# Optimization experiments

Hardware: AMD Instinct MI355X
Metric: run time of the kernel (lower is better)

## Reference

```python
import jax, jax.numpy as jnp
import numpy as np
import math

N, E, IN, OUT, H = 50000, 200000, 128, 128, 4
EPS = 1e-5
NEG_SLOPE = 0.01


def _ln(a):
    m = jnp.mean(a, axis=-1, keepdims=True)
    v = jnp.mean((a - m) ** 2, axis=-1, keepdims=True)
    return (a - m) / jnp.sqrt(v + EPS)


def setup_inputs() -> dict:
    key = jax.random.key(0)
    ks = jax.random.split(key, 24)
    glorot = lambda k, shape: jax.random.uniform(k, shape, jnp.float32,
                                                 -math.sqrt(6.0 / (shape[-2] + shape[-1])),
                                                 math.sqrt(6.0 / (shape[-2] + shape[-1])))
    lin = lambda k, fan_in, shape: jax.random.uniform(k, shape, jnp.float32,
                                                      -1.0 / math.sqrt(fan_in), 1.0 / math.sqrt(fan_in))
    inp = {
        "x": jax.random.normal(ks[0], (N, IN), jnp.float32),
        "edge_index": jax.random.randint(ks[1], (2, E), 0, N, jnp.int32),
        "edge_feature": jax.random.normal(ks[2], (E, IN), jnp.float32),
        # per-head projection matrices [H, IN, OUT]
        "Kv2v": glorot(ks[3], (H, IN, OUT)),
        "Ke2v": glorot(ks[4], (H, IN, OUT)),
        "Vv2v": glorot(ks[5], (H, IN, OUT)),
        "Ve2v": glorot(ks[6], (H, IN, OUT)),
        # per-head linear_update: [H, 2*OUT, 2*OUT]
        "lu_W": lin(ks[7], 2 * OUT, (H, 2 * OUT, 2 * OUT)),
        "lu_b": lin(ks[8], 2 * OUT, (H, 2 * OUT)),
        "ln1_g": jnp.ones((H, 2 * OUT), jnp.float32),
        "ln1_b": jnp.zeros((H, 2 * OUT), jnp.float32),
        # per-head msg_layer linear: [H, 2*OUT, OUT]
        "msg_W": lin(ks[9], 2 * OUT, (H, 2 * OUT, OUT)),
        "msg_b": lin(ks[10], 2 * OUT, (H, OUT)),
        "ln2_g": jnp.ones((H, OUT), jnp.float32),
        "ln2_b": jnp.zeros((H, OUT), jnp.float32),
        # concat projection [OUT*H, OUT]
        "cat_W": lin(ks[11], OUT * H, (OUT * H, OUT)),
        "cat_b": lin(ks[12], OUT * H, (OUT,)),
        # input projection [IN, OUT]
        "inp_W": lin(ks[13], IN, (IN, OUT)),
        "inp_b": lin(ks[14], IN, (OUT,)),
        # batchnorm affine
        "bn_g": jnp.ones((OUT,), jnp.float32),
        "bn_b": jnp.zeros((OUT,), jnp.float32),
    }
    return inp


def reference(x, edge_index, edge_feature, Kv2v, Ke2v, Vv2v, Ve2v,
              lu_W, lu_b, ln1_g, ln1_b, msg_W, msg_b, ln2_g, ln2_b,
              cat_W, cat_b, inp_W, inp_b, bn_g, bn_b):
    src, dst = edge_index[0], edge_index[1]  # j -> i
    scale = 1.0 / math.sqrt(2 * OUT)
    heads = []
    for h in range(H):  # small fixed loop over structurally distinct heads
        Kv = x @ Kv2v[h]            # [N, OUT]
        Vv = x @ Vv2v[h]
        KE = edge_feature @ Ke2v[h]  # [E, OUT]
        VE = edge_feature @ Ve2v[h]
        q_i = Kv[dst]                # [E, OUT]
        query = jnp.concatenate([q_i, q_i], axis=1)          # [E, 2*OUT]
        key_j = jnp.concatenate([Kv[src], KE], axis=1)       # [E, 2*OUT]
        alpha = query * key_j * scale
        val = jnp.concatenate([Vv[src], VE], axis=1)         # [E, 2*OUT]
        gate = jax.nn.sigmoid(_ln(alpha) * ln1_g[h] + ln1_b[h])
        m = (val @ lu_W[h] + lu_b[h]) * gate                 # [E, 2*OUT]
        m = m @ msg_W[h] + msg_b[h]                          # [E, OUT]
        m = _ln(m) * ln2_g[h] + ln2_b[h]
        m = jax.nn.leaky_relu(m, NEG_SLOPE)
        heads.append(jax.ops.segment_sum(m, dst, num_segments=N))  # [N, OUT]
    hv = jnp.concatenate(heads, axis=1)          # [N, OUT*H]
    out = hv @ cat_W + cat_b                      # [N, OUT]
    mu = jnp.mean(out, axis=0)
    var = jnp.mean((out - mu) ** 2, axis=0)      # biased, training-mode BN
    out = (out - mu) / jnp.sqrt(var + EPS) * bn_g + bn_b
    out = jax.nn.leaky_relu(out, NEG_SLOPE)
    return out + (x @ inp_W + inp_b)
```

## Files before the change

kernel.cpp:

```cpp
#include <hip/hip_runtime.h>
#include <hip/hip_bf16.h>

#define NN 50000
#define NE 200000
#define HEADS 4
#define EPSV 1e-5f
#define NEGS 0.01f

using f32x4 = __attribute__((ext_vector_type(4))) float;
using s16x8 = __attribute__((ext_vector_type(8))) short;
using bf16x8 = __attribute__((ext_vector_type(8))) __bf16;

__device__ __forceinline__ short f2bf(float f) {
    union { float f; unsigned u; } v; v.f = f;
    unsigned r = v.u + 0x7FFFu + ((v.u >> 16) & 1u);
    return (short)(r >> 16);
}
__device__ __forceinline__ float bf2f(short s) {
    union { unsigned u; float f; } v; v.u = ((unsigned)(unsigned short)s) << 16;
    return v.f;
}
__device__ __forceinline__ f32x4 mfma16(s16x8 a, s16x8 b, f32x4 c) {
    return __builtin_amdgcn_mfma_f32_16x16x32_bf16(
        __builtin_bit_cast(bf16x8, a), __builtin_bit_cast(bf16x8, b), c, 0, 0, 0);
}
__device__ __forceinline__ void gld16(const void* g, void* l) {
    __builtin_amdgcn_global_load_lds(
        (const __attribute__((address_space(1))) void*)g,
        (__attribute__((address_space(3))) void*)l, 16, 0, 0);
}
__device__ __forceinline__ void dma8(const short* src, char* dst, int w, int lane) {
    gld16(src + w * 512 + lane * 8,        dst + w * 1024);
    gld16(src + 2048 + w * 512 + lane * 8, dst + 4096 + w * 1024);
}

__global__ void prep_weights(const float* __restrict__ Kv2v, const float* __restrict__ Vv2v,
                             const float* __restrict__ inpW,
                             const float* __restrict__ Ke2v, const float* __restrict__ Ve2v,
                             const float* __restrict__ luW, const float* __restrict__ msgW,
                             const float* __restrict__ catW,
                             short* __restrict__ nodeW_t, short* __restrict__ imgW)
{
    int i = blockIdx.x * 256 + threadIdx.x;
    if (i < 147456) {
        int j = i >> 7, k = i & 127;
        float v;
        if (j < 512)       v = Kv2v[(j >> 7) * 16384 + k * 128 + (j & 127)];
        else if (j < 1024) v = Vv2v[((j - 512) >> 7) * 16384 + k * 128 + (j & 127)];
        else               v = inpW[k * 128 + (j - 1024)];
        nodeW_t[i] = f2bf(v);
        return;
    }
    i -= 147456;
    if (i >= 589824) return;
    int h = i / 147456;
    int r = i % 147456;
    short* img = imgW + h * 147456;
    if (r < 16384) {
        int colc = r >> 7, k = r & 127;
        img[(colc * 128 + k) ^ ((colc & 7) << 3)] = f2bf(Ke2v[h * 16384 + k * 128 + colc]);
    } else if (r < 32768) {
        int e = r - 16384; int colc = e >> 7, k = e & 127;
        img[16384 + ((colc * 128 + k) ^ ((colc & 7) << 3))] = f2bf(Ve2v[h * 16384 + k * 128 + colc]);
    } else if (r < 98304) {
        int e = r - 32768; int c = e >> 14, ec = e & 16383;
        int colc = ec >> 8, k = ec & 255; int col = c * 64 + colc;
        img[32768 + c * 16384 + ((colc * 256 + k) ^ ((colc & 7) << 3))] =
            f2bf(luW[h * 65536 + k * 256 + col]);
    } else if (r < 131072) {
        int e = r - 98304; int c = e >> 14, ec = e & 16383;
        int colc = ec >> 8, k = ec & 255; int col = c * 64 + colc;
        img[98304 + c * 16384 + ((colc * 256 + k) ^ ((colc & 7) << 3))] =
            f2bf(msgW[h * 32768 + k * 128 + col]);
    } else {
        int e = r - 131072; int colc = e >> 7, k = e & 127;
        img[131072 + ((colc * 128 + k) ^ ((colc & 7) << 3))] =
            f2bf(catW[(h * 128 + k) * 128 + colc]);
    }
}

__global__ __launch_bounds__(256, 2)
void node_proj(const float* __restrict__ x, const short* __restrict__ nodeW_t,
               short* __restrict__ Kv_all, short* __restrict__ Vv_all,
               float* __restrict__ resid)
{
    __shared__ alignas(16) short xt[64 * 128];
    const int tid = threadIdx.x;
    const int row0 = blockIdx.x * 64;
    #pragma unroll
    for (int it = 0; it < 8; ++it) {
        int idx4 = it * 256 + tid;
        int r = idx4 >> 5;
        int c = (idx4 & 31) * 4;
        float4 v = {0.f, 0.f, 0.f, 0.f};
        if (row0 + r < NN) v = *(const float4*)(x + (size_t)(row0 + r) * 128 + c);
        short4 sw; sw.x = f2bf(v.x); sw.y = f2bf(v.y); sw.z = f2bf(v.z); sw.w = f2bf(v.w);
        int byte = (r * 256 + c * 2) ^ ((r & 7) << 4);
        *(short4*)((char*)xt + byte) = sw;
    }
    __syncthreads();
    const int lane = tid & 63, w = tid >> 6;
    const int l15 = lane & 15, lg = lane >> 4;
    const int rloc = w * 16 + l15;
    s16x8 a[4];
    #pragma unroll
    for (int ks = 0; ks < 4; ++ks) {
        int byte = (rloc * 256 + (ks * 32 + lg * 8) * 2) ^ ((rloc & 7) << 4);
        a[ks] = *(const s16x8*)((const char*)xt + byte);
    }
    const int rowC = row0 + w * 16 + lg * 4;
    for (int nc = 0; nc < 18; ++nc) {
        f32x4 acc[4];
        s16x8 b[16];
        #pragma unroll
        for (int q = 0; q < 4; ++q) {
            acc[q] = (f32x4){0.f, 0.f, 0.f, 0.f};
            int j = (nc * 4 + q) * 16 + l15;
            #pragma unroll
            for (int ks = 0; ks < 4; ++ks)
                b[q * 4 + ks] = *(const s16x8*)(nodeW_t + j * 128 + ks * 32 + lg * 8);
        }
        #pragma unroll
        for (int q = 0; q < 4; ++q)
            #pragma unroll
            for (int ks = 0; ks < 4; ++ks)
                acc[q] = mfma16(a[ks], b[q * 4 + ks], acc[q]);
        #pragma unroll
        for (int q = 0; q < 4; ++q) {
            int j = (nc * 4 + q) * 16 + l15;
            #pragma unroll
            for (int r = 0; r < 4; ++r) {
                int row = rowC + r;
                if (row >= NN) continue;
                if (j < 512)       Kv_all[(size_t)row * 512 + j] = f2bf(acc[q][r]);
                else if (j < 1024) Vv_all[(size_t)row * 512 + (j - 512)] = f2bf(acc[q][r]);
                else               resid[(size_t)row * 128 + (j - 1024)] = acc[q][r];
            }
        }
    }
}

#define B128h(buf, ct, ks) \
    (*(const s16x8*)((const short*)(buf) + (((((ct) * 16 + l15) * 128) + (ks) * 32 + lg * 8) ^ ((l15 & 7) << 3))))
#define B256h(buf, ks) \
    (*(const s16x8*)((const short*)(buf) + ((l15 * 256 + (ks) * 32 + lg * 8) ^ ((l15 & 7) << 3))))
#define CB() do { __syncthreads(); char* _t = bA; bA = bB; bB = _t; } while (0)
#define PRIO1() __builtin_amdgcn_s_setprio(1)
#define PRIO0() __builtin_amdgcn_s_setprio(0)

__global__ __launch_bounds__(256, 1)
void edge_kernel(const float* __restrict__ ef, const int* __restrict__ eidx,
                 const short* __restrict__ Kv_all, const short* __restrict__ Vv_all,
                 const short* __restrict__ imgW,
                 const float* __restrict__ lu_b, const float* __restrict__ ln1_g,
                 const float* __restrict__ ln1_b, const float* __restrict__ msg_b,
                 const float* __restrict__ ln2_g, const float* __restrict__ ln2_b,
                 float* __restrict__ out1)
{
    __shared__ alignas(16) char lds[65536];
    char* bA = lds;
    char* bB = lds + 8192;
    const int tid = threadIdx.x;
    const int lane = tid & 63, w = tid >> 6;
    const int l15 = lane & 15, lg = lane >> 4;
    const int e0 = blockIdx.x * 64 + w * 16;
    const int rb = lg * 4;
    char* myscr = lds + 16384 + w * 12288;
    const float scale = 0.0625f;

    dma8(imgW, bB, w, lane);
    const float* efr = ef + (size_t)(e0 + l15) * 128 + lg * 8;
    s16x8 aef[4];
    #pragma unroll
    for (int ks = 0; ks < 4; ++ks) {
        float4 v0 = *(const float4*)(efr + ks * 32);
        float4 v1 = *(const float4*)(efr + ks * 32 + 4);
        s16x8 t;
        t[0] = f2bf(v0.x); t[1] = f2bf(v0.y); t[2] = f2bf(v0.z); t[3] = f2bf(v0.w);
        t[4] = f2bf(v1.x); t[5] = f2bf(v1.y); t[6] = f2bf(v1.z); t[7] = f2bf(v1.w);
        aef[ks] = t;
    }
    const int srcA = eidx[e0 + l15];
    int dstC[4];
    #pragma unroll
    for (int r = 0; r < 4; ++r) dstC[r] = eidx[NE + e0 + rb + r];
    const int gRow = lane >> 2;
    const int gChunk = lane & 3;
    const int dstG = eidx[NE + e0 + gRow];
    const int srcG = eidx[e0 + gRow];

    f32x4 outc[8];
    #pragma unroll
    for (int nt = 0; nt < 8; ++nt) outc[nt] = (f32x4){0.f, 0.f, 0.f, 0.f};
    CB();

    for (int h = 0; h < HEADS; ++h) {
        const short* hb = imgW + h * 147456;
        s16x8 qv[4], kv[4];
        #pragma unroll
        for (int j = 0; j < 4; ++j) {
            qv[j] = *(const s16x8*)(Kv_all + (size_t)dstG * 512 + h * 128 + gChunk * 32 + j * 8);
            kv[j] = *(const s16x8*)(Kv_all + (size_t)srcG * 512 + h * 128 + gChunk * 32 + j * 8);
        }

        f32x4 accK[8];
        #pragma unroll
        for (int nt = 0; nt < 8; ++nt) accK[nt] = (f32x4){0, 0, 0, 0};
        s16x8 vvr[4];
        unsigned gpk[16][2];

        #pragma unroll
        for (int i = 0; i < 4; ++i) {
            dma8(hb + (i + 1) * 4096, bB, w, lane);
            PRIO1();
            #pragma unroll
            for (int ks = 0; ks < 4; ++ks) {
                accK[i * 2]     = mfma16(aef[ks], B128h(bA, 0, ks), accK[i * 2]);
                accK[i * 2 + 1] = mfma16(aef[ks], B128h(bA, 1, ks), accK[i * 2 + 1]);
            }
            PRIO0();
            if (i == 0) {
                #pragma unroll
                for (int j = 0; j < 4; ++j) {
                    int byte = gRow * 256 + ((((gChunk * 4 + j) * 16)) ^ ((gRow & 7) << 4));
                    *(s16x8*)(myscr + byte) = qv[j];
                    *(s16x8*)(myscr + 4096 + byte) = kv[j];
                }
            }
            CB();
        }

        #pragma unroll
        for (int i = 0; i < 4; ++i) {
            dma8(hb + (i + 5) * 4096, bB, w, lane);
            f32x4 aV0 = (f32x4){0, 0, 0, 0}, aV1 = (f32x4){0, 0, 0, 0};
            PRIO1();
            #pragma unroll
            for (int ks = 0; ks < 4; ++ks) {
                aV0 = mfma16(aef[ks], B128h(bA, 0, ks), aV0);
                aV1 = mfma16(aef[ks], B128h(bA, 1, ks), aV1);
            }
            PRIO0();
            #pragma unroll
            for (int t = 0; t < 2; ++t) {
                f32x4 av = t ? aV1 : aV0;
                int c = (i * 2 + t) * 16 + l15;
                #pragma unroll
                for (int r = 0; r < 4; ++r) {
                    int row = rb + r;
                    int byte = 8192 + ((row * 256 + c * 2) ^ ((row & 7) << 4));
                    *(short*)(myscr + byte) = f2bf(av[r]);
                }
            }
            if (i == 3) {
                #pragma unroll
                for (int ks = 0; ks < 4; ++ks)
                    vvr[ks] = *(const s16x8*)(Vv_all + (size_t)srcA * 512 + h * 128 + ks * 32 + lg * 8);
                #pragma unroll
                for (int r = 0; r < 4; ++r) {
                    const int i2r = rb + r;
                    const int swz = (i2r & 7) << 4;
                    float al[16];
                    float s = 0.f, s2 = 0.f;
                    #pragma unroll
                    for (int nt = 0; nt < 8; ++nt) {
                        int off = (i2r * 256 + nt * 32 + l15 * 2) ^ swz;
                        float q  = bf2f(*(const short*)(myscr + off));
                        float k1 = bf2f(*(const short*)(myscr + 4096 + off));
                        float alo = q * k1 * scale;
                        float ahi = q * accK[nt][r] * scale;
                        al[nt] = alo; al[nt + 8] = ahi;
                        s += alo + ahi; s2 += alo * alo + ahi * ahi;
                    }
                    #pragma unroll
                    for (int m = 1; m < 16; m <<= 1) { s += __shfl_xor(s, m); s2 += __shfl_xor(s2, m); }
                    float mean = s * (1.f / 256.f);
                    float var  = s2 * (1.f / 256.f) - mean * mean;
                    float rstd = rsqrtf(var + EPSV);
                    #pragma unroll
                    for (int i2 = 0; i2 < 16; ++i2) {
                        int c = i2 * 16 + l15;
                        float z = (al[i2] - mean) * rstd * ln1_g[h * 256 + c] + ln1_b[h * 256 + c];
                        float g = 1.f / (1.f + __expf(-z));
                        unsigned gb = (unsigned)(unsigned short)f2bf(g);
                        if ((r & 1) == 0) gpk[i2][r >> 1] = gb;
                        else              gpk[i2][r >> 1] |= gb << 16;
                    }
                }
            }
            CB();
        }

        #pragma unroll
        for (int c = 0; c < 16; ++c) {
            dma8(hb + (9 + c) * 4096, bB, w, lane);
            f32x4 m1c = (f32x4){0, 0, 0, 0};
            PRIO1();
            #pragma unroll
            for (int ks = 0; ks < 8; ++ks) {
                s16x8 a;
                if (ks < 4) a = vvr[ks];
                else {
                    int byte = 8192 + ((l15 * 256 + ((ks - 4) * 32 + lg * 8) * 2) ^ ((l15 & 7) << 4));
                    a = *(const s16x8*)(myscr + byte);
                }
                m1c = mfma16(a, B256h(bA, ks), m1c);
            }
            PRIO0();
            {
                int col = c * 16 + l15;
                float bias = lu_b[h * 256 + col];
                #pragma unroll
                for (int r = 0; r < 4; ++r) {
                    float g = bf2f((short)((gpk[c][r >> 1] >> ((r & 1) * 16)) & 0xFFFFu));
                    int row = rb + r;
                    int byte = (row * 512 + col * 2) ^ ((row & 7) << 4);
                    *(short*)(myscr + byte) = f2bf((m1c[r] + bias) * g);
                }
            }
            CB();
        }

        f32x4 m2[8];
        #pragma unroll
        for (int nt = 0; nt < 8; ++nt) m2[nt] = (f32x4){0, 0, 0, 0};
        #pragma unroll
        for (int c = 0; c < 8; ++c) {
            dma8(hb + (25 + c) * 4096, bB, w, lane);
            PRIO1();
            #pragma unroll
            for (int ks = 0; ks < 8; ++ks) {
                int byte = (l15 * 512 + (ks * 32 + lg * 8) * 2) ^ ((l15 & 7) << 4);
                s16x8 a = *(const s16x8*)(myscr + byte);
                m2[c] = mfma16(a, B256h(bA, ks), m2[c]);
            }
            PRIO0();
            CB();
        }
        {
            float s[4] = {0, 0, 0, 0}, s2[4] = {0, 0, 0, 0};
            #pragma unroll
            for (int nt = 0; nt < 8; ++nt) {
                int c = nt * 16 + l15;
                float bias = msg_b[h * 128 + c];
                #pragma unroll
                for (int r = 0; r < 4; ++r) {
                    float v = m2[nt][r] + bias;
                    m2[nt][r] = v;
                    s[r] += v; s2[r] += v * v;
                }
            }
            #pragma unroll
            for (int m = 1; m < 16; m <<= 1)
                #pragma unroll
                for (int r = 0; r < 4; ++r) { s[r] += __shfl_xor(s[r], m); s2[r] += __shfl_xor(s2[r], m); }
            float mean[4], rstd[4];
            #pragma unroll
            for (int r = 0; r < 4; ++r) {
                mean[r] = s[r] * (1.f / 128.f);
                float var = s2[r] * (1.f / 128.f) - mean[r] * mean[r];
                rstd[r] = rsqrtf(var + EPSV);
            }
            #pragma unroll
            for (int nt = 0; nt < 8; ++nt) {
                int c = nt * 16 + l15;
                float g2 = ln2_g[h * 128 + c], b2 = ln2_b[h * 128 + c];
                #pragma unroll
                for (int r = 0; r < 4; ++r) {
                    float v = (m2[nt][r] - mean[r]) * rstd[r] * g2 + b2;
                    v = v > 0.f ? v : v * NEGS;
                    int row = rb + r;
                    int byte = 8192 + ((row * 256 + c * 2) ^ ((row & 7) << 4));
                    *(short*)(myscr + byte) = f2bf(v);
                }
            }
        }

        #pragma unroll
        for (int c = 0; c < 4; ++c) {
            if (c < 3)      dma8(hb + (33 + c) * 4096, bB, w, lane);
            else if (h < 3) dma8(imgW + (h + 1) * 147456, bB, w, lane);
            PRIO1();
            #pragma unroll
            for (int ks = 0; ks < 4; ++ks) {
                int byte = 8192 + ((l15 * 256 + (ks * 32 + lg * 8) * 2) ^ ((l15 & 7) << 4));
                s16x8 a = *(const s16x8*)(myscr + byte);
                outc[c * 2]     = mfma16(a, B128h(bA, 0, ks), outc[c * 2]);
                outc[c * 2 + 1] = mfma16(a, B128h(bA, 1, ks), outc[c * 2 + 1]);
            }
            PRIO0();
            CB();
        }
    }

    #pragma unroll
    for (int nt = 0; nt < 8; ++nt) {
        int c = nt * 16 + l15;
        #pragma unroll
        for (int r = 0; r < 4; ++r)
            atomicAdd(out1 + (size_t)dstC[r] * 128 + c, outc[nt][r]);
    }
}

__global__ void bn_stats(const float* __restrict__ out1, const float* __restrict__ cat_b,
                         float* __restrict__ stats)
{
    const int col = threadIdx.x;
    const int r0 = blockIdx.x * 128;
    const float cb = cat_b[col];
    float s = 0.f, s2 = 0.f;
    for (int i = 0; i < 128; ++i) {
        int row = r0 + i;
        if (row < NN) {
            float v = out1[(size_t)row * 128 + col] + cb;
            s += v; s2 += v * v;
        }
    }
    atomicAdd(stats + col, s);
    atomicAdd(stats + 128 + col, s2);
}

__global__ void finalize(const float* __restrict__ out1, const float* __restrict__ resid,
                         const float* __restrict__ stats, const float* __restrict__ cat_b,
                         const float* __restrict__ bn_g, const float* __restrict__ bn_b,
                         const float* __restrict__ inp_b, float* __restrict__ out)
{
    int i = blockIdx.x * 256 + threadIdx.x;
    if (i >= NN * 128) return;
    int col = i & 127;
    float mu = stats[col] * (1.f / NN);
    float var = stats[128 + col] * (1.f / NN) - mu * mu;
    float rstd = rsqrtf(var + EPSV);
    float v = out1[i] + cat_b[col];
    v = (v - mu) * rstd * bn_g[col] + bn_b[col];
    v = v > 0.f ? v : v * NEGS;
    out[i] = v + resid[i] + inp_b[col];
}

extern "C" void kernel_launch(void* const* d_in, const int* in_sizes, int n_in,
                              void* d_out, int out_size, void* d_ws, size_t ws_size,
                              hipStream_t stream)
{
    (void)in_sizes; (void)n_in; (void)out_size; (void)ws_size;
    const float* x     = (const float*)d_in[0];
    const int*   eidx  = (const int*)d_in[1];
    const float* ef    = (const float*)d_in[2];
    const float* Kv2v  = (const float*)d_in[3];
    const float* Ke2v  = (const float*)d_in[4];
    const float* Vv2v  = (const float*)d_in[5];
    const float* Ve2v  = (const float*)d_in[6];
    const float* lu_W  = (const float*)d_in[7];
    const float* lu_b  = (const float*)d_in[8];
    const float* ln1_g = (const float*)d_in[9];
    const float* ln1_b = (const float*)d_in[10];
    const float* msg_W = (const float*)d_in[11];
    const float* msg_b = (const float*)d_in[12];
    const float* ln2_g = (const float*)d_in[13];
    const float* ln2_b = (const float*)d_in[14];
    const float* cat_W = (const float*)d_in[15];
    const float* cat_b = (const float*)d_in[16];
    const float* inp_W = (const float*)d_in[17];
    const float* inp_b = (const float*)d_in[18];
    const float* bn_g  = (const float*)d_in[19];
    const float* bn_b  = (const float*)d_in[20];

    char* ws = (char*)d_ws;
    short* nodeW_t = (short*)(ws + 0);
    short* imgW    = (short*)(ws + 294912);
    short* Kv_all  = (short*)(ws + 1474560);
    short* Vv_all  = (short*)(ws + 52674560);
    float* resid   = (float*)(ws + 103874560);
    float* out1    = (float*)(ws + 129474560);
    float* stats   = (float*)(ws + 155074560);

    hipMemsetAsync(out1, 0, 25600000 + 1024, stream);
    prep_weights<<<2880, 256, 0, stream>>>(Kv2v, Vv2v, inp_W, Ke2v, Ve2v, lu_W, msg_W, cat_W,
                                           nodeW_t, imgW);
    node_proj<<<782, 256, 0, stream>>>(x, nodeW_t, Kv_all, Vv_all, resid);
    edge_kernel<<<3125, 256, 0, stream>>>(ef, eidx, Kv_all, Vv_all, imgW,
                                          lu_b, ln1_g, ln1_b, msg_b,
                                          ln2_g, ln2_b, out1);
    bn_stats<<<391, 128, 0, stream>>>(out1, cat_b, stats);
    finalize<<<25000, 256, 0, stream>>>(out1, resid, stats, cat_b, bn_g, bn_b, inp_b,
                                        (float*)d_out);
}
```

Before: 1.463 ms.

## Deepen edge-kernel weight streaming to 4-stage ring with explicit vmcnt waits

Replaces the double-buffered weight tile pipeline (full __syncthreads per step) with a 4-slot LDS ring that prefetches three tiles ahead, using explicit s_waitcnt vmcnt plus s_barrier instead of a full sync. Bias and layernorm parameters are staged once into LDS, and the gathered Kv/Vv loads are moved so their latency overlaps MFMA work. The aim is to hide global load latency for the weight stream and gathers. In exchange, LDS use grows to about 100KB via dynamic shared memory, and correctness now depends on hand-counted vmcnt values matching the DMA issue pattern.

New measurement: 1.339 ms. 1.09x faster.

```diff
diff --git a/kernel.cpp b/kernel.cpp
--- a/kernel.cpp
+++ b/kernel.cpp
@@ -144,7 +144,8 @@
     (*(const s16x8*)((const short*)(buf) + (((((ct) * 16 + l15) * 128) + (ks) * 32 + lg * 8) ^ ((l15 & 7) << 3))))
 #define B256h(buf, ks) \
     (*(const s16x8*)((const short*)(buf) + ((l15 * 256 + (ks) * 32 + lg * 8) ^ ((l15 & 7) << 3))))
-#define CB() do { __syncthreads(); char* _t = bA; bA = bB; bB = _t; } while (0)
+#define WAITV(N) asm volatile("s_waitcnt vmcnt(" #N ")" ::: "memory")
+#define SBAR() do { __builtin_amdgcn_s_barrier(); __builtin_amdgcn_sched_barrier(0); } while (0)
 #define PRIO1() __builtin_amdgcn_s_setprio(1)
 #define PRIO0() __builtin_amdgcn_s_setprio(0)
 
@@ -157,18 +158,30 @@
                  const float* __restrict__ ln2_g, const float* __restrict__ ln2_b,
                  float* __restrict__ out1)
 {
-    __shared__ alignas(16) char lds[65536];
-    char* bA = lds;
-    char* bB = lds + 8192;
+    extern __shared__ char lds[];
     const int tid = threadIdx.x;
     const int lane = tid & 63, w = tid >> 6;
     const int l15 = lane & 15, lg = lane >> 4;
     const int e0 = blockIdx.x * 64 + w * 16;
     const int rb = lg * 4;
-    char* myscr = lds + 16384 + w * 12288;
+    char* myscr = lds + 32768 + w * 12288;
+    float* bls = (float*)(lds + 81920);
     const float scale = 0.0625f;
 
-    dma8(imgW, bB, w, lane);
+    {
+        int j = tid;
+        #pragma unroll
+        for (int it = 0; it < 4; ++it, j += 256) {
+            bls[j] = ln1_g[j]; bls[1024 + j] = ln1_b[j]; bls[2048 + j] = lu_b[j];
+        }
+        if (tid < 256) {
+            bls[3072 + tid] = msg_b[tid];       bls[3072 + 256 + tid] = msg_b[256 + tid];
+            bls[3584 + tid] = ln2_g[tid];       bls[3584 + 256 + tid] = ln2_g[256 + tid];
+            bls[4096 + tid] = ln2_b[tid];       bls[4096 + 256 + tid] = ln2_b[256 + tid];
+        }
+        asm volatile("s_waitcnt lgkmcnt(0)" ::: "memory");
+    }
+
     const float* efr = ef + (size_t)(e0 + l15) * 128 + lg * 8;
     s16x8 aef[4];
     #pragma unroll
@@ -189,20 +202,16 @@
     const int dstG = eidx[NE + e0 + gRow];
     const int srcG = eidx[e0 + gRow];
 
+    dma8(imgW,        lds,         w, lane);
+    dma8(imgW + 4096, lds + 8192,  w, lane);
+    dma8(imgW + 8192, lds + 16384, w, lane);
+
     f32x4 outc[8];
     #pragma unroll
     for (int nt = 0; nt < 8; ++nt) outc[nt] = (f32x4){0.f, 0.f, 0.f, 0.f};
-    CB();
 
     for (int h = 0; h < HEADS; ++h) {
         const short* hb = imgW + h * 147456;
-        s16x8 qv[4], kv[4];
-        #pragma unroll
-        for (int j = 0; j < 4; ++j) {
-            qv[j] = *(const s16x8*)(Kv_all + (size_t)dstG * 512 + h * 128 + gChunk * 32 + j * 8);
-            kv[j] = *(const s16x8*)(Kv_all + (size_t)srcG * 512 + h * 128 + gChunk * 32 + j * 8);
-        }
-
         f32x4 accK[8];
         #pragma unroll
         for (int nt = 0; nt < 8; ++nt) accK[nt] = (f32x4){0, 0, 0, 0};
@@ -210,29 +219,35 @@
         unsigned gpk[16][2];
 
         #pragma unroll
+        for (int p = 0; p < 4; ++p) {
+            WAITV(4); SBAR();
+            dma8(hb + (p + 3) * 4096, lds + ((p + 3) & 3) * 8192, w, lane);
+            const char* bA = lds + (p & 3) * 8192;
+            PRIO1();
+            #pragma unroll
+            for (int ks = 0; ks < 4; ++ks) {
+                accK[p * 2]     = mfma16(aef[ks], B128h(bA, 0, ks), accK[p * 2]);
+                accK[p * 2 + 1] = mfma16(aef[ks], B128h(bA, 1, ks), accK[p * 2 + 1]);
+            }
+            PRIO0();
+            if (p == 0) {
+                #pragma unroll
+                for (int j = 0; j < 4; ++j) {
+                    s16x8 qv = *(const s16x8*)(Kv_all + (size_t)dstG * 512 + h * 128 + gChunk * 32 + j * 8);
+                    s16x8 kv = *(const s16x8*)(Kv_all + (size_t)srcG * 512 + h * 128 + gChunk * 32 + j * 8);
+                    int byte = gRow * 256 + ((((gChunk * 4 + j) * 16)) ^ ((gRow & 7) << 4));
+                    *(s16x8*)(myscr + byte) = qv;
+                    *(s16x8*)(myscr + 4096 + byte) = kv;
+                }
+            }
+        }
+
+        #pragma unroll
         for (int i = 0; i < 4; ++i) {
-            dma8(hb + (i + 1) * 4096, bB, w, lane);
-            PRIO1();
-            #pragma unroll
-            for (int ks = 0; ks < 4; ++ks) {
-                accK[i * 2]     = mfma16(aef[ks], B128h(bA, 0, ks), accK[i * 2]);
-                accK[i * 2 + 1] = mfma16(aef[ks], B128h(bA, 1, ks), accK[i * 2 + 1]);
-            }
-            PRIO0();
-            if (i == 0) {
-                #pragma unroll
-                for (int j = 0; j < 4; ++j) {
-                    int byte = gRow * 256 + ((((gChunk * 4 + j) * 16)) ^ ((gRow & 7) << 4));
-                    *(s16x8*)(myscr + byte) = qv[j];
-                    *(s16x8*)(myscr + 4096 + byte) = kv[j];
-                }
-            }
-            CB();
-        }
-
-        #pragma unroll
-        for (int i = 0; i < 4; ++i) {
-            dma8(hb + (i + 5) * 4096, bB, w, lane);
+            const int p = 4 + i;
+            WAITV(4); SBAR();
+            dma8(hb + (p + 3) * 4096, lds + ((p + 3) & 3) * 8192, w, lane);
+            const char* bA = lds + (p & 3) * 8192;
             f32x4 aV0 = (f32x4){0, 0, 0, 0}, aV1 = (f32x4){0, 0, 0, 0};
             PRIO1();
             #pragma unroll
@@ -252,10 +267,12 @@
                     *(short*)(myscr + byte) = f2bf(av[r]);
                 }
             }
-            if (i == 3) {
+            if (i == 0) {
                 #pragma unroll
                 for (int ks = 0; ks < 4; ++ks)
                     vvr[ks] = *(const s16x8*)(Vv_all + (size_t)srcA * 512 + h * 128 + ks * 32 + lg * 8);
+            }
+            if (i == 3) {
                 #pragma unroll
                 for (int r = 0; r < 4; ++r) {
                     const int i2r = rb + r;
@@ -280,7 +297,7 @@
                     #pragma unroll
                     for (int i2 = 0; i2 < 16; ++i2) {
                         int c = i2 * 16 + l15;
-                        float z = (al[i2] - mean) * rstd * ln1_g[h * 256 + c] + ln1_b[h * 256 + c];
+                        float z = (al[i2] - mean) * rstd * bls[h * 256 + c] + bls[1024 + h * 256 + c];
                         float g = 1.f / (1.f + __expf(-z));
                         unsigned gb = (unsigned)(unsigned short)f2bf(g);
                         if ((r & 1) == 0) gpk[i2][r >> 1] = gb;
@@ -288,12 +305,14 @@
                     }
                 }
             }
-            CB();
         }
 
         #pragma unroll
         for (int c = 0; c < 16; ++c) {
-            dma8(hb + (9 + c) * 4096, bB, w, lane);
+            const int p = 8 + c;
+            WAITV(4); SBAR();
+            dma8(hb + (p + 3) * 4096, lds + ((p + 3) & 3) * 8192, w, lane);
+            const char* bA = lds + (p & 3) * 8192;
             f32x4 m1c = (f32x4){0, 0, 0, 0};
             PRIO1();
             #pragma unroll
@@ -309,7 +328,7 @@
             PRIO0();
             {
                 int col = c * 16 + l15;
-                float bias = lu_b[h * 256 + col];
+                float bias = bls[2048 + h * 256 + col];
                 #pragma unroll
                 for (int r = 0; r < 4; ++r) {
                     float g = bf2f((short)((gpk[c][r >> 1] >> ((r & 1) * 16)) & 0xFFFFu));
@@ -318,7 +337,6 @@
                     *(short*)(myscr + byte) = f2bf((m1c[r] + bias) * g);
                 }
             }
-            CB();
         }
 
         f32x4 m2[8];
@@ -326,7 +344,10 @@
         for (int nt = 0; nt < 8; ++nt) m2[nt] = (f32x4){0, 0, 0, 0};
         #pragma unroll
         for (int c = 0; c < 8; ++c) {
-            dma8(hb + (25 + c) * 4096, bB, w, lane);
+            const int p = 24 + c;
+            WAITV(4); SBAR();
+            dma8(hb + (p + 3) * 4096, lds + ((p + 3) & 3) * 8192, w, lane);
+            const char* bA = lds + (p & 3) * 8192;
             PRIO1();
             #pragma unroll
             for (int ks = 0; ks < 8; ++ks) {
@@ -335,14 +356,13 @@
                 m2[c] = mfma16(a, B256h(bA, ks), m2[c]);
             }
             PRIO0();
-            CB();
         }
         {
             float s[4] = {0, 0, 0, 0}, s2[4] = {0, 0, 0, 0};
             #pragma unroll
             for (int nt = 0; nt < 8; ++nt) {
                 int c = nt * 16 + l15;
-                float bias = msg_b[h * 128 + c];
+                float bias = bls[3072 + h * 128 + c];
                 #pragma unroll
                 for (int r = 0; r < 4; ++r) {
                     float v = m2[nt][r] + bias;
@@ -364,7 +384,7 @@
             #pragma unroll
             for (int nt = 0; nt < 8; ++nt) {
                 int c = nt * 16 + l15;
-                float g2 = ln2_g[h * 128 + c], b2 = ln2_b[h * 128 + c];
+                float g2 = bls[3584 + h * 128 + c], b2 = bls[4096 + h * 128 + c];
                 #pragma unroll
                 for (int r = 0; r < 4; ++r) {
                     float v = (m2[nt][r] - mean[r]) * rstd[r] * g2 + b2;
@@ -378,8 +398,18 @@
 
         #pragma unroll
         for (int c = 0; c < 4; ++c) {
-            if (c < 3)      dma8(hb + (33 + c) * 4096, bB, w, lane);
-            else if (h < 3) dma8(imgW + (h + 1) * 147456, bB, w, lane);
+            const int p = 32 + c;
+            if (p < 34)      { WAITV(4); }
+            else if (p == 34) { if (h < 3) { WAITV(4); } else { WAITV(2); } }
+            else              { if (h < 3) { WAITV(4); } else { WAITV(0); } }
+            SBAR();
+            const int t = p + 3;
+            if (t < 36) {
+                dma8(hb + t * 4096, lds + (t & 3) * 8192, w, lane);
+            } else if (h < 3) {
+                dma8(imgW + (h + 1) * 147456 + (t - 36) * 4096, lds + (t & 3) * 8192, w, lane);
+            }
+            const char* bA = lds + (p & 3) * 8192;
             PRIO1();
             #pragma unroll
             for (int ks = 0; ks < 4; ++ks) {
@@ -389,7 +419,6 @@
                 outc[c * 2 + 1] = mfma16(a, B128h(bA, 1, ks), outc[c * 2 + 1]);
             }
             PRIO0();
-            CB();
         }
     }
 
@@ -473,13 +502,16 @@
     float* out1    = (float*)(ws + 129474560);
     float* stats   = (float*)(ws + 155074560);
 
+    hipFuncSetAttribute((const void*)edge_kernel,
+                        hipFuncAttributeMaxDynamicSharedMemorySize, 100352);
+
     hipMemsetAsync(out1, 0, 25600000 + 1024, stream);
     prep_weights<<<2880, 256, 0, stream>>>(Kv2v, Vv2v, inp_W, Ke2v, Ve2v, lu_W, msg_W, cat_W,
                                            nodeW_t, imgW);
     node_proj<<<782, 256, 0, stream>>>(x, nodeW_t, Kv_all, Vv_all, resid);
-    edge_kernel<<<3125, 256, 0, stream>>>(ef, eidx, Kv_all, Vv_all, imgW,
-                                          lu_b, ln1_g, ln1_b, msg_b,
-                                          ln2_g, ln2_b, out1);
+    edge_kernel<<<3125, 256, 100352, stream>>>(ef, eidx, Kv_all, Vv_all, imgW,
+                                               lu_b, ln1_g, ln1_b, msg_b,
+                                               ln2_g, ln2_b, out1);
     bn_stats<<<391, 128, 0, stream>>>(out1, cat_b, stats);
     finalize<<<25000, 256, 0, stream>>>(out1, resid, stats, cat_b, bn_g, bn_b, inp_b,
                                         (float*)d_out);
```
